# Kernel tuning notes

Measured on AMD Instinct MI355X. Metric: run time of the kernel, lower is better.

Reference implementation:

```python
import jax, jax.numpy as jnp
import numpy as np
import math

NUM_HEADS = 32
NUM_KV_HEADS = 8
HEAD_DIM = 64
ROPE_THETA = 150000.0


def rotate_half(x):
    half = x.shape[-1] // 2
    return jnp.concatenate([-x[..., half:], x[..., :half]], axis=-1)


def setup_inputs() -> dict:
    key = jax.random.key(0)
    k1, k2, k3, k4, k5 = jax.random.split(key, 5)
    B, S, H = 2, 2048, 2048
    qkv_size = (NUM_HEADS + 2 * NUM_KV_HEADS) * HEAD_DIM  # 3072
    scale = 1.0 / math.sqrt(H)
    return {
        "hidden_states": jax.random.normal(k1, (B, S, H), jnp.float32),
        "position_ids": jnp.arange(S, dtype=jnp.int64 if jax.config.jax_enable_x64 else jnp.int32)[None, :],
        "qkv_w": jax.random.normal(k2, (qkv_size, H), jnp.float32) * scale,
        "qkv_b": jax.random.normal(k3, (qkv_size,), jnp.float32) * 0.01,
        "o_w": jax.random.normal(k4, (H, NUM_HEADS * HEAD_DIM), jnp.float32) * scale,
        "o_b": jax.random.normal(k5, (H,), jnp.float32) * 0.01,
    }


def reference(hidden_states, position_ids, qkv_w, qkv_b, o_w, o_b):
    B, S, _ = hidden_states.shape
    g = NUM_HEADS // NUM_KV_HEADS  # query heads per kv head
    d = HEAD_DIM

    qkv = hidden_states @ qkv_w.T + qkv_b  # [B,S,(H+2KV)*d]
    qkv = qkv.reshape(B, S, NUM_KV_HEADS, g + 2, d)
    q = qkv[:, :, :, :g, :].reshape(B, S, NUM_HEADS, d).transpose(0, 2, 1, 3)   # [B,Hq,S,d]
    k = qkv[:, :, :, g, :].transpose(0, 2, 1, 3)                                 # [B,Hkv,S,d]
    v = qkv[:, :, :, g + 1, :].transpose(0, 2, 1, 3)                             # [B,Hkv,S,d]

    # HF-style RoPE: cos/sin [S, d]
    inv_freq = 1.0 / (ROPE_THETA ** (jnp.arange(0, d, 2, dtype=jnp.float32) / d))
    freqs = jnp.outer(position_ids.reshape(-1).astype(jnp.float32), inv_freq)    # [S, d/2]
    emb = jnp.concatenate([freqs, freqs], axis=-1)                               # [S, d]
    cos = jnp.cos(emb)[None, None]                                               # [1,1,S,d]
    sin = jnp.sin(emb)[None, None]
    q = q * cos + rotate_half(q) * sin
    k = k * cos + rotate_half(k) * sin

    # GQA: repeat_interleave kv heads to match query heads
    k = jnp.repeat(k, g, axis=1)  # [B,Hq,S,d]
    v = jnp.repeat(v, g, axis=1)

    scores = jnp.einsum("bhqd,bhkd->bhqk", q, k) / math.sqrt(d)  # [B,Hq,S,S]
    attn = jax.nn.softmax(scores, axis=-1)
    out = jnp.einsum("bhqk,bhkd->bhqd", attn, v)
    out = out.transpose(0, 2, 1, 3).reshape(B, S, NUM_HEADS * d)
    return out @ o_w.T + o_b
```

## Files before the change

kernel.cpp:

```cpp
#include <hip/hip_runtime.h>
#include <math.h>

#define NHQ 32
#define NKV 8
#define HD 64
#define QKV_DIM 3072
#define MODEL_DIM 2048
#define QSCALE 0.1803368801111204f

typedef __attribute__((ext_vector_type(4))) float     f32x4;
typedef __attribute__((ext_vector_type(8))) _Float16  half8;
typedef __attribute__((ext_vector_type(4))) _Float16  half4v;
typedef __attribute__((ext_vector_type(2))) __fp16    fp16x2;

#define ASYNC_COPY16(g, l)                                                        \
    __builtin_amdgcn_global_load_lds(                                             \
        (const __attribute__((address_space(1))) void*)(g),                       \
        (__attribute__((address_space(3))) void*)(l), 16, 0, 0)

__device__ __forceinline__ float fast_exp2(float x)
{
#if __has_builtin(__builtin_amdgcn_exp2f)
    return __builtin_amdgcn_exp2f(x);
#else
    float r;
    asm volatile("v_exp_f32 %0, %1\ns_nop 0" : "=v"(r) : "v"(x));
    return r;
#endif
}

__global__ __launch_bounds__(256)
void setup_kernel(const float* __restrict__ ha, const float* __restrict__ hb,
                  const float* __restrict__ hc, _Float16* __restrict__ da,
                  _Float16* __restrict__ db, _Float16* __restrict__ dc,
                  const int* __restrict__ pos, float* __restrict__ tab,
                  int n4a, int n4b, int n4c, int S)
{
    int i = blockIdx.x * 256 + threadIdx.x;
    if (i < n4a + n4b + n4c) {
        const float* src; _Float16* dst; int j;
        if (i < n4a)            { src = ha; dst = da; j = i; }
        else if (i < n4a + n4b) { src = hb; dst = db; j = i - n4a; }
        else                    { src = hc; dst = dc; j = i - n4a - n4b; }
        float4 v = ((const float4*)src)[j];
        half4v h = { (_Float16)v.x, (_Float16)v.y, (_Float16)v.z, (_Float16)v.w };
        ((half4v*)dst)[j] = h;
    } else {
        int k = i - (n4a + n4b + n4c);
        if (k < S * 32) {
            int s = k >> 5, fi = k & 31;
            float p = (float)pos[s];
            float inv_freq = powf(150000.0f, -(float)fi * (1.0f / 32.0f));
            float ang = p * inv_freq;
            tab[s * 64 + fi]      = cosf(ang);
            tab[s * 64 + 32 + fi] = sinf(ang);
        }
    }
}

template<int MODE>
__global__ __launch_bounds__(256)
void gemm_f16_mfma(const _Float16* __restrict__ A, const _Float16* __restrict__ W,
                   const float* __restrict__ bias, void* __restrict__ Cout,
                   const float* __restrict__ tab, int M, int N, int K, int S)
{
    __shared__ _Float16 As[128 * 32];
    __shared__ _Float16 Bs[128 * 32];

    const int t    = threadIdx.x;
    const int w    = t >> 6;
    const int lane = t & 63;
    const int quad = lane >> 4, l15 = lane & 15;
    const size_t m0 = (size_t)blockIdx.y * 128;
    const size_t n0 = (size_t)blockIdx.x * 128;
    const int wm = (w >> 1) * 64, wn = (w & 1) * 64;

    const int row0 = t >> 2;
    const int sub  = (t & 3) * 8;
    const _Float16* ag0 = A + (m0 + row0) * K + sub;
    const _Float16* ag1 = A + (m0 + 64 + row0) * K + sub;
    const _Float16* bg0 = W + (n0 + row0) * K + sub;
    const _Float16* bg1 = W + (n0 + 64 + row0) * K + sub;
    _Float16* al0 = &As[w * 512];
    _Float16* al1 = &As[2048 + w * 512];
    _Float16* bl0 = &Bs[w * 512];
    _Float16* bl1 = &Bs[2048 + w * 512];

    f32x4 acc[4][4];
#pragma unroll
    for (int i = 0; i < 4; i++)
#pragma unroll
        for (int j = 0; j < 4; j++) acc[i][j] = (f32x4){0.f, 0.f, 0.f, 0.f};

    for (int k0 = 0; k0 < K; k0 += 32) {
        ASYNC_COPY16(ag0 + k0, al0);
        ASYNC_COPY16(ag1 + k0, al1);
        ASYNC_COPY16(bg0 + k0, bl0);
        ASYNC_COPY16(bg1 + k0, bl1);
        __syncthreads();

        half8 af[4], bf[4];
#pragma unroll
        for (int i = 0; i < 4; i++) {
            af[i] = *(const half8*)&As[(wm + i * 16 + l15) * 32 + quad * 8];
            bf[i] = *(const half8*)&Bs[(wn + i * 16 + l15) * 32 + quad * 8];
        }
#pragma unroll
        for (int i = 0; i < 4; i++)
#pragma unroll
            for (int j = 0; j < 4; j++)
                acc[i][j] = __builtin_amdgcn_mfma_f32_16x16x32_f16(af[i], bf[j], acc[i][j], 0, 0, 0);
        __syncthreads();
    }

    float bv[4];
#pragma unroll
    for (int j = 0; j < 4; j++) bv[j] = bias[n0 + wn + j * 16 + l15];

    const int ct = (int)(((n0 + wn) >> 6) % 6);

#pragma unroll
    for (int i = 0; i < 4; i++)
#pragma unroll
        for (int r = 0; r < 4; r++) {
            const size_t row = m0 + wm + i * 16 + quad * 4 + r;
            float v[4];
#pragma unroll
            for (int j = 0; j < 4; j++) v[j] = acc[i][j][r] + bv[j];

            if (MODE == 2 && ct != 5) {
                const float* tc = tab + (size_t)(row % S) * 64;
                const float ca = tc[l15],      sa = tc[32 + l15];
                const float cb = tc[16 + l15], sb = tc[48 + l15];
                const float qs = (ct < 4) ? QSCALE : 1.0f;
                const float n0v = v[0] * ca - v[2] * sa;
                const float n1v = v[1] * cb - v[3] * sb;
                const float n2v = v[2] * ca + v[0] * sa;
                const float n3v = v[3] * cb + v[1] * sb;
                v[0] = n0v * qs; v[1] = n1v * qs; v[2] = n2v * qs; v[3] = n3v * qs;
            }

            const size_t col = n0 + wn + l15;
#pragma unroll
            for (int j = 0; j < 4; j++) {
                if (MODE != 0) ((_Float16*)Cout)[row * N + col + j * 16] = (_Float16)v[j];
                else           ((float*)Cout)[row * N + col + j * 16] = v[j];
            }
        }
}

__global__ __launch_bounds__(256)
void transpose_v_kernel(const _Float16* __restrict__ qkv, _Float16* __restrict__ vtg, int BS)
{
    __shared__ _Float16 tile[64 * 72];
    const int t = threadIdx.x;
    const int tb = blockIdx.x * 64;
    const int g = blockIdx.y;
    const int voff = (g * 6 + 5) * 64;

    const int tok = t >> 2, dsub = (t & 3) * 16;
    const _Float16* src = qkv + (size_t)(tb + tok) * QKV_DIM + voff + dsub;
    *(half8*)&tile[tok * 72 + dsub]     = *(const half8*)(src);
    *(half8*)&tile[tok * 72 + dsub + 8] = *(const half8*)(src + 8);
    __syncthreads();

    const int d = t >> 2, tsub = (t & 3) * 16;
    half8 a, c;
#pragma unroll
    for (int i = 0; i < 8; i++) a[i] = tile[(tsub + i) * 72 + d];
#pragma unroll
    for (int i = 0; i < 8; i++) c[i] = tile[(tsub + 8 + i) * 72 + d];
    _Float16* dst = vtg + ((size_t)g * 64 + d) * BS + tb + tsub;
    *(half8*)dst       = a;
    *(half8*)(dst + 8) = c;
}

__global__ __launch_bounds__(256)
void attn_mfma(const _Float16* __restrict__ qkv, const _Float16* __restrict__ vtg,
               _Float16* __restrict__ out, int B, int S)
{
    __shared__ _Float16 KP[4 * 32 * 72];
    __shared__ _Float16 VsT[80 * 72];

    const int t = threadIdx.x, w = t >> 6, lane = t & 63;
    const int quad = lane >> 4, l15 = lane & 15;
    const int b = blockIdx.z, g = blockIdx.y;
    const int q0 = blockIdx.x * 32;
    const int qoff = (g * 6 + w) * 64;
    const int koff = (g * 6 + 4) * 64;

    _Float16* Ps = &KP[w * 2304];

    half8 qf[2][2];
#pragma unroll
    for (int s = 0; s < 2; s++) {
        const _Float16* qp = qkv + (size_t)(b * S + q0 + s * 16 + l15) * QKV_DIM + qoff;
        qf[s][0] = *(const half8*)(qp + quad * 8);
        qf[s][1] = *(const half8*)(qp + 32 + quad * 8);
    }

    for (int idx = 64 * 72 + t; idx < 80 * 72; idx += 256)
        VsT[idx] = (idx < 65 * 72) ? (_Float16)1.0f : (_Float16)0.0f;

    f32x4 O[2][4], L[2];
#pragma unroll
    for (int s = 0; s < 2; s++) {
        L[s] = (f32x4){0.f, 0.f, 0.f, 0.f};
#pragma unroll
        for (int dt = 0; dt < 4; dt++) O[s][dt] = (f32x4){0.f, 0.f, 0.f, 0.f};
    }

    const int kst_tok = t >> 2;
    const int kst_d   = (t & 3) * 16;
    const int vst_d   = t >> 3;
    const int vst_sub = (t & 7) * 8;

    const _Float16* kbase  = qkv + (size_t)(b * S + kst_tok) * QKV_DIM + koff + kst_d;
    const _Float16* vbase0 = vtg + ((size_t)g * 64 + vst_d) * (size_t)(B * S) + b * S + vst_sub;
    const _Float16* vbase1 = vtg + ((size_t)g * 64 + 32 + vst_d) * (size_t)(B * S) + b * S + vst_sub;

    half8 kr0 = *(const half8*)(kbase);
    half8 kr1 = *(const half8*)(kbase + 8);
    half8 vr0 = *(const half8*)(vbase0);
    half8 vr1 = *(const half8*)(vbase1);

    for (int kt = 0; kt < S; kt += 64) {
        *(half8*)&KP[kst_tok * 72 + kst_d]      = kr0;
        *(half8*)&KP[kst_tok * 72 + kst_d + 8]  = kr1;
        *(half8*)&VsT[vst_d * 72 + vst_sub]        = vr0;
        *(half8*)&VsT[(32 + vst_d) * 72 + vst_sub] = vr1;
        __syncthreads();

        if (kt + 64 < S) {
            kr0 = *(const half8*)(kbase + (size_t)(kt + 64) * QKV_DIM);
            kr1 = *(const half8*)(kbase + (size_t)(kt + 64) * QKV_DIM + 8);
            vr0 = *(const half8*)(vbase0 + kt + 64);
            vr1 = *(const half8*)(vbase1 + kt + 64);
        }

        half8 kf[4][2];
#pragma unroll
        for (int mt = 0; mt < 4; mt++) {
            kf[mt][0] = *(const half8*)&KP[(mt * 16 + l15) * 72 + quad * 8];
            kf[mt][1] = *(const half8*)&KP[(mt * 16 + l15) * 72 + 32 + quad * 8];
        }
        f32x4 sacc[2][4];
#pragma unroll
        for (int s = 0; s < 2; s++)
#pragma unroll
            for (int mt = 0; mt < 4; mt++) {
                f32x4 z = (f32x4){0.f, 0.f, 0.f, 0.f};
                z = __builtin_amdgcn_mfma_f32_16x16x32_f16(kf[mt][0], qf[s][0], z, 0, 0, 0);
                z = __builtin_amdgcn_mfma_f32_16x16x32_f16(kf[mt][1], qf[s][1], z, 0, 0, 0);
                sacc[s][mt] = z;
            }
        __syncthreads();

#pragma unroll
        for (int s = 0; s < 2; s++)
#pragma unroll
            for (int mt = 0; mt < 4; mt++) {
                fp16x2 pa = __builtin_amdgcn_cvt_pkrtz(fast_exp2(sacc[s][mt][0]),
                                                       fast_exp2(sacc[s][mt][1]));
                fp16x2 pb = __builtin_amdgcn_cvt_pkrtz(fast_exp2(sacc[s][mt][2]),
                                                       fast_exp2(sacc[s][mt][3]));
                uint2 u;
                u.x = __builtin_bit_cast(unsigned int, pa);
                u.y = __builtin_bit_cast(unsigned int, pb);
                *(uint2*)&Ps[(s * 16 + l15) * 72 + mt * 16 + quad * 4] = u;
            }
        asm volatile("s_waitcnt lgkmcnt(0)" ::: "memory");

        half8 pf[2][2];
#pragma unroll
        for (int s = 0; s < 2; s++) {
            pf[s][0] = *(const half8*)&Ps[(s * 16 + l15) * 72 + quad * 8];
            pf[s][1] = *(const half8*)&Ps[(s * 16 + l15) * 72 + 32 + quad * 8];
        }
#pragma unroll
        for (int dt = 0; dt < 4; dt++) {
            half8 vv0 = *(const half8*)&VsT[(dt * 16 + l15) * 72 + quad * 8];
            half8 vv1 = *(const half8*)&VsT[(dt * 16 + l15) * 72 + 32 + quad * 8];
#pragma unroll
            for (int s = 0; s < 2; s++) {
                O[s][dt] = __builtin_amdgcn_mfma_f32_16x16x32_f16(pf[s][0], vv0, O[s][dt], 0, 0, 0);
                O[s][dt] = __builtin_amdgcn_mfma_f32_16x16x32_f16(pf[s][1], vv1, O[s][dt], 0, 0, 0);
            }
        }
        {
            half8 lv0 = *(const half8*)&VsT[(64 + l15) * 72 + quad * 8];
            half8 lv1 = *(const half8*)&VsT[(64 + l15) * 72 + 32 + quad * 8];
#pragma unroll
            for (int s = 0; s < 2; s++) {
                L[s] = __builtin_amdgcn_mfma_f32_16x16x32_f16(pf[s][0], lv0, L[s], 0, 0, 0);
                L[s] = __builtin_amdgcn_mfma_f32_16x16x32_f16(pf[s][1], lv1, L[s], 0, 0, 0);
            }
        }
        __syncthreads();
    }

    const int hq = g * 4 + w;
#pragma unroll
    for (int s = 0; s < 2; s++)
#pragma unroll
        for (int r = 0; r < 4; r++) {
            const float lr = __shfl(L[s][r], lane & 48, 64);
            const float ir = 1.0f / lr;
            const size_t row = (size_t)(b * S + q0 + s * 16 + quad * 4 + r);
#pragma unroll
            for (int dt = 0; dt < 4; dt++)
                out[row * (NHQ * HD) + hq * 64 + dt * 16 + l15] = (_Float16)(O[s][dt][r] * ir);
        }
}

extern "C" void kernel_launch(void* const* d_in, const int* in_sizes, int n_in,
                              void* d_out, int out_size, void* d_ws, size_t ws_size,
                              hipStream_t stream)
{
    const float* hidden = (const float*)d_in[0];
    const int*   pos    = (const int*)d_in[1];
    const float* qkv_w  = (const float*)d_in[2];
    const float* qkv_b  = (const float*)d_in[3];
    const float* o_w    = (const float*)d_in[4];
    const float* o_b    = (const float*)d_in[5];
    float* out = (float*)d_out;

    const int S  = in_sizes[1];
    const int BS = in_sizes[0] / MODEL_DIM;
    const int B  = BS / S;

    _Float16* hA   = (_Float16*)d_ws;
    _Float16* hW1  = hA   + (size_t)BS * MODEL_DIM;
    _Float16* hW2  = hW1  + (size_t)QKV_DIM * MODEL_DIM;
    _Float16* qkvh = hW2  + (size_t)MODEL_DIM * MODEL_DIM;
    _Float16* atth = qkvh + (size_t)BS * QKV_DIM;
    float*    tab  = (float*)(atth + (size_t)BS * MODEL_DIM);
    _Float16* vtg  = (_Float16*)(tab + (size_t)S * 64);

    const int n4a = BS * MODEL_DIM / 4;
    const int n4b = QKV_DIM * MODEL_DIM / 4;
    const int n4c = MODEL_DIM * MODEL_DIM / 4;
    const int setup_items = n4a + n4b + n4c + S * 32;

    setup_kernel<<<(setup_items + 255) / 256, 256, 0, stream>>>(
        hidden, qkv_w, o_w, hA, hW1, hW2, pos, tab, n4a, n4b, n4c, S);

    gemm_f16_mfma<2><<<dim3(QKV_DIM / 128, BS / 128), 256, 0, stream>>>(
        hA, hW1, qkv_b, qkvh, tab, BS, QKV_DIM, MODEL_DIM, S);

    transpose_v_kernel<<<dim3(BS / 64, NKV), 256, 0, stream>>>(qkvh, vtg, BS);

    attn_mfma<<<dim3(S / 32, NKV, B), 256, 0, stream>>>(qkvh, vtg, atth, B, S);

    gemm_f16_mfma<0><<<dim3(MODEL_DIM / 128, BS / 128), 256, 0, stream>>>(
        atth, hW2, o_b, out, nullptr, BS, MODEL_DIM, MODEL_DIM, S);
}
```

Measured before the change: 350.2 us.

## Load K/V fragments directly from global memory in attention, drop LDS staging and barriers

```diff
diff --git a/kernel.cpp b/kernel.cpp
--- a/kernel.cpp
+++ b/kernel.cpp
@@ -179,17 +179,17 @@
 void attn_mfma(const _Float16* __restrict__ qkv, const _Float16* __restrict__ vtg,
                _Float16* __restrict__ out, int B, int S)
 {
-    __shared__ _Float16 KP[4 * 32 * 72];
-    __shared__ _Float16 VsT[80 * 72];
+    __shared__ _Float16 PsAll[4][32 * 72];
 
     const int t = threadIdx.x, w = t >> 6, lane = t & 63;
     const int quad = lane >> 4, l15 = lane & 15;
-    const int b = blockIdx.z, g = blockIdx.y;
-    const int q0 = blockIdx.x * 32;
+    const int g = blockIdx.x, b = blockIdx.z;
+    const int q0 = blockIdx.y * 32;
     const int qoff = (g * 6 + w) * 64;
     const int koff = (g * 6 + 4) * 64;
-
-    _Float16* Ps = &KP[w * 2304];
+    const size_t BSz = (size_t)B * S;
+
+    _Float16* Ps = &PsAll[w][0];
 
     half8 qf[2][2];
 #pragma unroll
@@ -199,8 +199,11 @@
         qf[s][1] = *(const half8*)(qp + 32 + quad * 8);
     }
 
-    for (int idx = 64 * 72 + t; idx < 80 * 72; idx += 256)
-        VsT[idx] = (idx < 65 * 72) ? (_Float16)1.0f : (_Float16)0.0f;
+    const _Float16* kfb = qkv + (size_t)(b * S + l15) * QKV_DIM + koff + quad * 8;
+    const _Float16* vfb = vtg + ((size_t)g * 64 + l15) * BSz + (size_t)b * S + quad * 8;
+
+    const half8 ones = { (_Float16)1.f, (_Float16)1.f, (_Float16)1.f, (_Float16)1.f,
+                         (_Float16)1.f, (_Float16)1.f, (_Float16)1.f, (_Float16)1.f };
 
     f32x4 O[2][4], L[2];
 #pragma unroll
@@ -210,65 +213,45 @@
         for (int dt = 0; dt < 4; dt++) O[s][dt] = (f32x4){0.f, 0.f, 0.f, 0.f};
     }
 
-    const int kst_tok = t >> 2;
-    const int kst_d   = (t & 3) * 16;
-    const int vst_d   = t >> 3;
-    const int vst_sub = (t & 7) * 8;
-
-    const _Float16* kbase  = qkv + (size_t)(b * S + kst_tok) * QKV_DIM + koff + kst_d;
-    const _Float16* vbase0 = vtg + ((size_t)g * 64 + vst_d) * (size_t)(B * S) + b * S + vst_sub;
-    const _Float16* vbase1 = vtg + ((size_t)g * 64 + 32 + vst_d) * (size_t)(B * S) + b * S + vst_sub;
-
-    half8 kr0 = *(const half8*)(kbase);
-    half8 kr1 = *(const half8*)(kbase + 8);
-    half8 vr0 = *(const half8*)(vbase0);
-    half8 vr1 = *(const half8*)(vbase1);
-
     for (int kt = 0; kt < S; kt += 64) {
-        *(half8*)&KP[kst_tok * 72 + kst_d]      = kr0;
-        *(half8*)&KP[kst_tok * 72 + kst_d + 8]  = kr1;
-        *(half8*)&VsT[vst_d * 72 + vst_sub]        = vr0;
-        *(half8*)&VsT[(32 + vst_d) * 72 + vst_sub] = vr1;
-        __syncthreads();
-
-        if (kt + 64 < S) {
-            kr0 = *(const half8*)(kbase + (size_t)(kt + 64) * QKV_DIM);
-            kr1 = *(const half8*)(kbase + (size_t)(kt + 64) * QKV_DIM + 8);
-            vr0 = *(const half8*)(vbase0 + kt + 64);
-            vr1 = *(const half8*)(vbase1 + kt + 64);
-        }
+        const _Float16* kp = kfb + (size_t)kt * QKV_DIM;
+        const _Float16* vp = vfb + kt;
 
         half8 kf[4][2];
 #pragma unroll
         for (int mt = 0; mt < 4; mt++) {
-            kf[mt][0] = *(const half8*)&KP[(mt * 16 + l15) * 72 + quad * 8];
-            kf[mt][1] = *(const half8*)&KP[(mt * 16 + l15) * 72 + 32 + quad * 8];
-        }
-        f32x4 sacc[2][4];
-#pragma unroll
-        for (int s = 0; s < 2; s++)
+            kf[mt][0] = *(const half8*)(kp + (size_t)(mt * 16) * QKV_DIM);
+            kf[mt][1] = *(const half8*)(kp + (size_t)(mt * 16) * QKV_DIM + 32);
+        }
+        half8 vv[4][2];
+#pragma unroll
+        for (int dt = 0; dt < 4; dt++) {
+            vv[dt][0] = *(const half8*)(vp + (size_t)(dt * 16) * BSz);
+            vv[dt][1] = *(const half8*)(vp + (size_t)(dt * 16) * BSz + 32);
+        }
+
+#pragma unroll
+        for (int s = 0; s < 2; s++) {
+            f32x4 sacc[4];
 #pragma unroll
             for (int mt = 0; mt < 4; mt++) {
                 f32x4 z = (f32x4){0.f, 0.f, 0.f, 0.f};
                 z = __builtin_amdgcn_mfma_f32_16x16x32_f16(kf[mt][0], qf[s][0], z, 0, 0, 0);
                 z = __builtin_amdgcn_mfma_f32_16x16x32_f16(kf[mt][1], qf[s][1], z, 0, 0, 0);
-                sacc[s][mt] = z;
-            }
-        __syncthreads();
-
-#pragma unroll
-        for (int s = 0; s < 2; s++)
+                sacc[mt] = z;
+            }
 #pragma unroll
             for (int mt = 0; mt < 4; mt++) {
-                fp16x2 pa = __builtin_amdgcn_cvt_pkrtz(fast_exp2(sacc[s][mt][0]),
-                                                       fast_exp2(sacc[s][mt][1]));
-                fp16x2 pb = __builtin_amdgcn_cvt_pkrtz(fast_exp2(sacc[s][mt][2]),
-                                                       fast_exp2(sacc[s][mt][3]));
+                fp16x2 pa = __builtin_amdgcn_cvt_pkrtz(fast_exp2(sacc[mt][0]),
+                                                       fast_exp2(sacc[mt][1]));
+                fp16x2 pb = __builtin_amdgcn_cvt_pkrtz(fast_exp2(sacc[mt][2]),
+                                                       fast_exp2(sacc[mt][3]));
                 uint2 u;
                 u.x = __builtin_bit_cast(unsigned int, pa);
                 u.y = __builtin_bit_cast(unsigned int, pb);
                 *(uint2*)&Ps[(s * 16 + l15) * 72 + mt * 16 + quad * 4] = u;
             }
+        }
         asm volatile("s_waitcnt lgkmcnt(0)" ::: "memory");
 
         half8 pf[2][2];
@@ -277,26 +260,19 @@
             pf[s][0] = *(const half8*)&Ps[(s * 16 + l15) * 72 + quad * 8];
             pf[s][1] = *(const half8*)&Ps[(s * 16 + l15) * 72 + 32 + quad * 8];
         }
-#pragma unroll
-        for (int dt = 0; dt < 4; dt++) {
-            half8 vv0 = *(const half8*)&VsT[(dt * 16 + l15) * 72 + quad * 8];
-            half8 vv1 = *(const half8*)&VsT[(dt * 16 + l15) * 72 + 32 + quad * 8];
+
+#pragma unroll
+        for (int dt = 0; dt < 4; dt++)
 #pragma unroll
             for (int s = 0; s < 2; s++) {
-                O[s][dt] = __builtin_amdgcn_mfma_f32_16x16x32_f16(pf[s][0], vv0, O[s][dt], 0, 0, 0);
-                O[s][dt] = __builtin_amdgcn_mfma_f32_16x16x32_f16(pf[s][1], vv1, O[s][dt], 0, 0, 0);
-            }
-        }
-        {
-            half8 lv0 = *(const half8*)&VsT[(64 + l15) * 72 + quad * 8];
-            half8 lv1 = *(const half8*)&VsT[(64 + l15) * 72 + 32 + quad * 8];
-#pragma unroll
-            for (int s = 0; s < 2; s++) {
-                L[s] = __builtin_amdgcn_mfma_f32_16x16x32_f16(pf[s][0], lv0, L[s], 0, 0, 0);
-                L[s] = __builtin_amdgcn_mfma_f32_16x16x32_f16(pf[s][1], lv1, L[s], 0, 0, 0);
-            }
-        }
-        __syncthreads();
+                O[s][dt] = __builtin_amdgcn_mfma_f32_16x16x32_f16(pf[s][0], vv[dt][0], O[s][dt], 0, 0, 0);
+                O[s][dt] = __builtin_amdgcn_mfma_f32_16x16x32_f16(pf[s][1], vv[dt][1], O[s][dt], 0, 0, 0);
+            }
+#pragma unroll
+        for (int s = 0; s < 2; s++) {
+            L[s] = __builtin_amdgcn_mfma_f32_16x16x32_f16(pf[s][0], ones, L[s], 0, 0, 0);
+            L[s] = __builtin_amdgcn_mfma_f32_16x16x32_f16(pf[s][1], ones, L[s], 0, 0, 0);
+        }
     }
 
     const int hq = g * 4 + w;
@@ -304,8 +280,7 @@
     for (int s = 0; s < 2; s++)
 #pragma unroll
         for (int r = 0; r < 4; r++) {
-            const float lr = __shfl(L[s][r], lane & 48, 64);
-            const float ir = 1.0f / lr;
+            const float ir = 1.0f / L[s][r];
             const size_t row = (size_t)(b * S + q0 + s * 16 + quad * 4 + r);
 #pragma unroll
             for (int dt = 0; dt < 4; dt++)
@@ -350,7 +325,7 @@
 
     transpose_v_kernel<<<dim3(BS / 64, NKV), 256, 0, stream>>>(qkvh, vtg, BS);
 
-    attn_mfma<<<dim3(S / 32, NKV, B), 256, 0, stream>>>(qkvh, vtg, atth, B, S);
+    attn_mfma<<<dim3(NKV, S / 32, B), 256, 0, stream>>>(qkvh, vtg, atth, B, S);
 
     gemm_f16_mfma<0><<<dim3(MODEL_DIM / 128, BS / 128), 256, 0, stream>>>(
         atth, hW2, o_b, out, nullptr, BS, MODEL_DIM, MODEL_DIM, S);
```

Measured after the change: 471.0 us. +34.5%, slower.
